# Kernel optimization log

Measured on AMD Instinct MI355X. Metric: run time of the kernel, lower is better.

Reference implementation:

```python
import jax, jax.numpy as jnp
import numpy as np

KERNEL = 16
STRIDE = 4


def setup_inputs() -> dict:
    key = jax.random.key(0)
    k1, k2 = jax.random.split(key)
    x = jax.random.normal(k1, (4096, 8192), dtype=jnp.float32)
    # nn.init.uniform_(Or_weight, 0.3, 0.7)
    w = 0.3 + 0.4 * jax.random.uniform(k2, (1, KERNEL), dtype=jnp.float32)
    return {"input": x, "Or_weight": w}


def _eventually(rho):
    # Soft "Eventually" (soft max) over the last axis: softmax-weighted average.
    return jnp.sum(rho * jax.nn.softmax(rho, axis=-1), axis=-1)


def reference(input, Or_weight):
    N, L = input.shape
    out_len = (L - KERNEL) // STRIDE + 1
    starts = jnp.arange(out_len) * STRIDE                      # [out_len]
    idx = starts[:, None] + jnp.arange(KERNEL)[None, :]        # [out_len, k]
    windows = input[:, idx]                                    # [N, out_len, k]
    rho = windows * Or_weight[0][None, None, :]                # [N, out_len, k]
    return _eventually(rho)                                    # [N, out_len]
```

## Files before the change

### kernel.cpp

```cpp
#include <hip/hip_runtime.h>

constexpr int KSZ     = 16;
constexpr int STRIDE  = 4;
constexpr int NROWS   = 4096;
constexpr int LCOLS   = 8192;
constexpr int OUT_LEN = (LCOLS - KSZ) / STRIDE + 1;
constexpr int BLOCK   = 512;
constexpr int NF4     = LCOLS / 4;

__device__ __forceinline__ int swz(int p) { return p ^ ((p >> 3) & 7); }

__global__ __launch_bounds__(BLOCK) void or_conv_kernel(
    const float* __restrict__ x, const float* __restrict__ w,
    float* __restrict__ out)
{
    __shared__ float4 smem[NF4];

    const int t = threadIdx.x;
    const int n = blockIdx.x;

    float wr[KSZ];
#pragma unroll
    for (int k = 0; k < KSZ; ++k) wr[k] = w[k];

    const float4* rowp4 = reinterpret_cast<const float4*>(x + (size_t)n * LCOLS);
#pragma unroll
    for (int j = 0; j < 4; ++j) {
        const int pos = t + BLOCK * j;
        smem[swz(pos)] = rowp4[pos];
    }
    __syncthreads();

    float* orow = out + (size_t)n * OUT_LEN;
#pragma unroll
    for (int i = 0; i < 4; ++i) {
        const int o = t + BLOCK * i;
        if (o < OUT_LEN) {
            float win[KSZ];
#pragma unroll
            for (int j = 0; j < 4; ++j) {
                const float4 v = smem[swz(o + j)];
                win[4 * j + 0] = v.x; win[4 * j + 1] = v.y;
                win[4 * j + 2] = v.z; win[4 * j + 3] = v.w;
            }
            float se = 0.f, sr = 0.f;
#pragma unroll
            for (int k = 0; k < KSZ; ++k) {
                const float rho = win[k] * wr[k];
                const float e   = __expf(rho);
                se += e;
                sr  = fmaf(rho, e, sr);
            }
            __builtin_nontemporal_store(sr * __builtin_amdgcn_rcpf(se), orow + o);
        }
    }
}

extern "C" void kernel_launch(void* const* d_in, const int* in_sizes, int n_in,
                              void* d_out, int out_size, void* d_ws, size_t ws_size,
                              hipStream_t stream)
{
    const float* x = (const float*)d_in[0];
    const float* w = (const float*)d_in[1];
    float* out     = (float*)d_out;

    or_conv_kernel<<<dim3(NROWS), dim3(BLOCK), 0, stream>>>(x, w, out);
}
```

Before: 32.36 us.

## Compute four consecutive outputs per thread from shared register window

Each thread now loads seven float4s (28 floats) once from shared memory and computes four adjacent outputs, instead of reloading four float4s for each of four strided outputs. The exp is rewritten as exp2 with the weights prescaled by log2(e), and the result is scaled back by ln2. The swizzle gains an extra XOR term to suit the new per-thread access pattern. This cuts LDS traffic and exp scaling work, at the cost of more registers and output stores that are no longer contiguous across threads or nontemporal.

```diff
diff --git a/kernel.cpp b/kernel.cpp
--- a/kernel.cpp
+++ b/kernel.cpp
@@ -8,7 +8,9 @@
 constexpr int BLOCK   = 512;
 constexpr int NF4     = LCOLS / 4;
 
-__device__ __forceinline__ int swz(int p) { return p ^ ((p >> 3) & 7); }
+__device__ __forceinline__ int swz(int q) {
+    return q ^ (((q >> 3) ^ (q >> 6)) & 7);
+}
 
 __global__ __launch_bounds__(BLOCK) void or_conv_kernel(
     const float* __restrict__ x, const float* __restrict__ w,
@@ -19,9 +21,9 @@
     const int t = threadIdx.x;
     const int n = blockIdx.x;
 
-    float wr[KSZ];
+    float wr2[KSZ];
 #pragma unroll
-    for (int k = 0; k < KSZ; ++k) wr[k] = w[k];
+    for (int k = 0; k < KSZ; ++k) wr2[k] = w[k] * 1.44269504089f;
 
     const float4* rowp4 = reinterpret_cast<const float4*>(x + (size_t)n * LCOLS);
 #pragma unroll
@@ -31,28 +33,32 @@
     }
     __syncthreads();
 
-    float* orow = out + (size_t)n * OUT_LEN;
+    float4 f[7];
+#pragma unroll
+    for (int j = 0; j < 7; ++j) {
+        const int q = min(4 * t + j, NF4 - 1);
+        f[j] = smem[swz(q)];
+    }
+    const float* win = reinterpret_cast<const float*>(f);
+
+    float res[4];
 #pragma unroll
     for (int i = 0; i < 4; ++i) {
-        const int o = t + BLOCK * i;
-        if (o < OUT_LEN) {
-            float win[KSZ];
+        float se = 0.f, sr = 0.f;
 #pragma unroll
-            for (int j = 0; j < 4; ++j) {
-                const float4 v = smem[swz(o + j)];
-                win[4 * j + 0] = v.x; win[4 * j + 1] = v.y;
-                win[4 * j + 2] = v.z; win[4 * j + 3] = v.w;
-            }
-            float se = 0.f, sr = 0.f;
+        for (int k = 0; k < KSZ; ++k) {
+            const float tt = win[STRIDE * i + k] * wr2[k];
+            const float e  = __builtin_amdgcn_exp2f(tt);
+            se += e;
+            sr  = fmaf(tt, e, sr);
+        }
+        res[i] = sr * 0.69314718056f * __builtin_amdgcn_rcpf(se);
+    }
+
+    float* op = out + (size_t)n * OUT_LEN + 4 * t;
 #pragma unroll
-            for (int k = 0; k < KSZ; ++k) {
-                const float rho = win[k] * wr[k];
-                const float e   = __expf(rho);
-                se += e;
-                sr  = fmaf(rho, e, sr);
-            }
-            __builtin_nontemporal_store(sr * __builtin_amdgcn_rcpf(se), orow + o);
-        }
+    for (int i = 0; i < 4; ++i) {
+        if (4 * t + i < OUT_LEN) op[i] = res[i];
     }
 }
 
```

Result: faster. 30.88 us (-4.6%).
